# Kernel optimization log

Measured on AMD Instinct MI355X. Metric: run time of the kernel, lower is better.

Reference implementation:

```python
import jax, jax.numpy as jnp
import numpy as np

B, S, D = 4, 2048, 1024
H = 16
DH = D // H


def setup_inputs() -> dict:
    key = jax.random.key(0)
    ks = jax.random.split(key, 9)
    s = 0.02
    return {
        "x": jax.random.normal(ks[0], (B, S, D), dtype=jnp.float32),
        "Wq": jax.random.normal(ks[1], (D, D), dtype=jnp.float32) * s,
        "bq": jax.random.normal(ks[2], (D,), dtype=jnp.float32) * s,
        "Wk": jax.random.normal(ks[3], (D, D), dtype=jnp.float32) * s,
        "bk": jax.random.normal(ks[4], (D,), dtype=jnp.float32) * s,
        "Wv": jax.random.normal(ks[5], (D, D), dtype=jnp.float32) * s,
        "bv": jax.random.normal(ks[6], (D,), dtype=jnp.float32) * s,
        "Wo": jax.random.normal(ks[7], (D, D), dtype=jnp.float32) * s,
        "bo": jax.random.normal(ks[8], (D,), dtype=jnp.float32) * s,
    }


def _split_heads(t):
    # [B,S,D] -> [B,H,S,DH]
    b, s, d = t.shape
    return t.reshape(b, s, H, DH).transpose(0, 2, 1, 3)


def reference(x, Wq, bq, Wk, bk, Wv, bv, Wo, bo):
    q = _split_heads(x @ Wq.T + bq)
    k = _split_heads(x @ Wk.T + bk)
    v = _split_heads(x @ Wv.T + bv)
    scale = 1.0 / np.sqrt(DH).astype(np.float32)
    scores = jnp.einsum("bhqd,bhkd->bhqk", q, k) * scale  # [B,H,S,S]
    s = scores.shape[-2]
    causal = jnp.tril(jnp.ones((s, s), dtype=bool))
    scores = jnp.where(causal[None, None], scores, -jnp.inf)
    probs = jax.nn.softmax(scores, axis=-1)
    out = jnp.einsum("bhqk,bhkd->bhqd", probs, v)  # [B,H,S,DH]
    out = out.transpose(0, 2, 1, 3).reshape(x.shape[0], s, D)
    return out @ Wo.T + bo
```

## Files before the change

kernel.cpp:

```cpp
#include <hip/hip_runtime.h>
#include <hip/hip_bf16.h>
#include <cstdint>
#include <cstddef>


typedef unsigned short u16;
typedef __bf16 bf16x8 __attribute__((ext_vector_type(8)));
typedef float  f32x4  __attribute__((ext_vector_type(4)));

__device__ __forceinline__ u16 f2bf(float f) {
  unsigned u = __float_as_uint(f);
  unsigned r = u + 0x7fffu + ((u >> 16) & 1u);
  return (u16)(r >> 16);
}

__device__ __forceinline__ void llds16(const u16* g, u16* l) {
  __builtin_amdgcn_global_load_lds(
      (const __attribute__((address_space(1))) void*)g,
      (__attribute__((address_space(3))) void*)l, 16, 0, 0);
}

__global__ void cast_bf16_kernel(const float* __restrict__ in, u16* __restrict__ out, int n4) {
  int i = blockIdx.x * blockDim.x + threadIdx.x;
  if (i >= n4) return;
  float4 f = ((const float4*)in)[i];
  ushort4 u;
  u.x = f2bf(f.x); u.y = f2bf(f.y); u.z = f2bf(f.z); u.w = f2bf(f.w);
  ((ushort4*)out)[i] = u;
}

__global__ void cast4_kernel(const float* __restrict__ a, const float* __restrict__ b,
                             const float* __restrict__ c, const float* __restrict__ d,
                             u16* __restrict__ oa, u16* __restrict__ ob,
                             u16* __restrict__ oc, u16* __restrict__ od, int n4) {
  const int w = blockIdx.y;
  const float* src = (w == 0) ? a : (w == 1) ? b : (w == 2) ? c : d;
  u16* dst = (w == 0) ? oa : (w == 1) ? ob : (w == 2) ? oc : od;
  int i = blockIdx.x * blockDim.x + threadIdx.x;
  if (i >= n4) return;
  float4 f = ((const float4*)src)[i];
  ushort4 u;
  u.x = f2bf(f.x); u.y = f2bf(f.y); u.z = f2bf(f.z); u.w = f2bf(f.w);
  ((ushort4*)dst)[i] = u;
}

__global__ __launch_bounds__(256) void gemm_bt(
    const u16* __restrict__ A, const u16* __restrict__ Bw,
    const float* __restrict__ b0, const float* __restrict__ b1, const float* __restrict__ b2,
    u16* __restrict__ qkv_out, float* __restrict__ flat_out,
    int K, int mode)
{
  __shared__ u16 As[128 * 32];
  __shared__ u16 Bs[128 * 32];

  const int tid = threadIdx.x;
  const int n0 = blockIdx.x * 128;
  const int m0 = blockIdx.y * 128;

  const int srow = tid >> 2;
  const int soff = (tid & 3) * 8;
  const u16* gA0 = A  + (size_t)(m0 + srow) * K + soff;
  const u16* gA1 = gA0 + (size_t)64 * K;
  const u16* gB0 = Bw + (size_t)(n0 + srow) * K + soff;
  const u16* gB1 = gB0 + (size_t)64 * K;
  u16* lA0 = As + tid * 8;
  u16* lA1 = As + 2048 + tid * 8;
  u16* lB0 = Bs + tid * 8;
  u16* lB1 = Bs + 2048 + tid * 8;

  const int lane = tid & 63;
  const int wave = tid >> 6;
  const int wm = (wave >> 1) * 64;
  const int wn = (wave & 1) * 64;
  const int fr = lane & 15;
  const int k8 = (lane >> 4) * 8;

  f32x4 zero = {0.f, 0.f, 0.f, 0.f};
  f32x4 acc[4][4];
#pragma unroll
  for (int i = 0; i < 4; i++)
#pragma unroll
    for (int j = 0; j < 4; j++) acc[i][j] = zero;

  for (int k0 = 0; k0 < K; k0 += 32) {
    llds16(gA0 + k0, lA0);
    llds16(gA1 + k0, lA1);
    llds16(gB0 + k0, lB0);
    llds16(gB1 + k0, lB1);
    __syncthreads();
    bf16x8 af[4], bfr[4];
#pragma unroll
    for (int i = 0; i < 4; i++)
      af[i] = *(const bf16x8*)(As + (wm + i * 16 + fr) * 32 + k8);
#pragma unroll
    for (int j = 0; j < 4; j++)
      bfr[j] = *(const bf16x8*)(Bs + (wn + j * 16 + fr) * 32 + k8);
#pragma unroll
    for (int i = 0; i < 4; i++)
#pragma unroll
      for (int j = 0; j < 4; j++)
        acc[i][j] = __builtin_amdgcn_mfma_f32_16x16x32_bf16(af[i], bfr[j], acc[i][j], 0, 0, 0);
    __syncthreads();
  }

  const int rbase = (lane >> 4) * 4;
  if (mode == 0) {
    const int which = n0 >> 10;
    const float* bias = (which == 0) ? b0 : ((which == 1) ? b1 : b2);
    const float post = (which == 0) ? 0.18033688011f : 1.0f;
    u16* outb = qkv_out + (size_t)which * 8388608;
#pragma unroll
    for (int j = 0; j < 4; j++) {
      const int nn = (n0 + wn + j * 16 + fr) & 1023;
      const float bb = bias[nn];
      const int h = nn >> 6, dh = nn & 63;
#pragma unroll
      for (int i = 0; i < 4; i++) {
#pragma unroll
        for (int r = 0; r < 4; r++) {
          const int m = m0 + wm + i * 16 + rbase + r;
          const int bI = m >> 11, s = m & 2047;
          outb[(((size_t)bI * 16 + h) * 2048 + s) * 64 + dh] = f2bf((acc[i][j][r] + bb) * post);
        }
      }
    }
  } else {
#pragma unroll
    for (int j = 0; j < 4; j++) {
      const int n = n0 + wn + j * 16 + fr;
      const float bb = b0[n];
#pragma unroll
      for (int i = 0; i < 4; i++) {
#pragma unroll
        for (int r = 0; r < 4; r++) {
          const int m = m0 + wm + i * 16 + rbase + r;
          flat_out[(size_t)m * 1024 + n] = acc[i][j][r] + bb;
        }
      }
    }
  }
}

__global__ __launch_bounds__(256) void transpose_v(const u16* __restrict__ V, u16* __restrict__ VT) {
  __shared__ u16 t_s[64 * 72];
  const int tid = threadIdx.x;
  const int st = blockIdx.x << 6;
  const int bh = blockIdx.y;
  const u16* src = V + ((size_t)bh * 2048 + st) * 64;
#pragma unroll
  for (int p = 0; p < 2; p++) {
    int i = p * 256 + tid;
    int row = i >> 3, ch = i & 7;
    bf16x8 v = *(const bf16x8*)(src + row * 64 + ch * 8);
    *(bf16x8*)(t_s + row * 72 + ch * 8) = v;
  }
  __syncthreads();
  u16* dst = VT + (size_t)bh * 131072 + st;
#pragma unroll
  for (int p = 0; p < 2; p++) {
    int i = p * 256 + tid;
    int dh = i >> 3, ch = i & 7;
    union { u16 s[8]; bf16x8 v; } u;
#pragma unroll
    for (int e = 0; e < 8; e++) u.s[e] = t_s[(ch * 8 + e) * 72 + dh];
    *(bf16x8*)(dst + (size_t)dh * 2048 + ch * 8) = u.v;
  }
}

__global__ __launch_bounds__(256, 2) void attn_fa(
    const u16* __restrict__ Qb, const u16* __restrict__ Kb,
    const u16* __restrict__ VT, u16* __restrict__ Ob)
{
  __shared__ u16 k_s[2 * 4096];
  __shared__ u16 v_s[2 * 4096];
  __shared__ u16 p_s[2 * 9216];
  __shared__ float l_s[256];

  const int tid = threadIdx.x;
  const int lane = tid & 63;
  const int wave = tid >> 6;

  const int c = (int)blockIdx.x;
  const int xcd = c & 7;
  const int rr_ = c >> 3;
  const int bh = xcd + ((rr_ >> 3) << 3);
  const int pr = rr_ & 7;
  const int qtA = pr;
  const int qtB = 15 - pr;

  const size_t head = (size_t)bh << 17;
  const int fr = lane & 15;
  const int g = lane >> 4;
  const int k8 = g << 3;
  const int q0A = qtA << 7;
  const int q0B = qtB << 7;
  const int wrow = wave << 5;

  bf16x8 aqA[2][2], aqB[2][2];
#pragma unroll
  for (int f = 0; f < 2; f++) {
    const u16* qpA = Qb + head + (size_t)(q0A + wrow + (f << 4) + fr) * 64;
    aqA[f][0] = *(const bf16x8*)(qpA + k8);
    aqA[f][1] = *(const bf16x8*)(qpA + 32 + k8);
    const u16* qpB = Qb + head + (size_t)(q0B + wrow + (f << 4) + fr) * 64;
    aqB[f][0] = *(const bf16x8*)(qpB + k8);
    aqB[f][1] = *(const bf16x8*)(qpB + 32 + k8);
  }

  const int r0 = tid >> 3, c0 = tid & 7;
  const int r1 = 32 + r0;
  const int koff0 = r0 * 64 + (((c0 ^ r0) & 7) << 3);
  const int koff1 = r1 * 64 + (((c0 ^ r1) & 7) << 3);
  const int voff0 = r0 * 2048 + (((c0 ^ r0) & 7) << 3);
  const int voff1 = r1 * 2048 + (((c0 ^ r1) & 7) << 3);
  int kaddr[4][2], vaddr[2][4];
#pragma unroll
  for (int j = 0; j < 4; j++) {
    const int kn = (j << 4) + fr;
    kaddr[j][0] = kn * 64 + (((g ^ kn) & 7) << 3);
    kaddr[j][1] = kn * 64 + ((((g + 4) ^ kn) & 7) << 3);
#pragma unroll
    for (int s2 = 0; s2 < 2; s2++)
      vaddr[s2][j] = kn * 64 + ((((s2 << 2) + g) ^ (kn & 7)) << 3);
  }
  u16* const prowA0 = p_s + (wrow + fr) * 72;
  u16* const prowA1 = p_s + (wrow + 16 + fr) * 72;
  u16* const prowB0 = p_s + 9216 + (wrow + fr) * 72;
  u16* const prowB1 = p_s + 9216 + (wrow + 16 + fr) * 72;
  const u16* Kbase = Kb + head;
  const u16* Vbase = VT + head;

  auto issueK = [&](int jt2, int buf) {
    const u16* Kt = Kbase + ((size_t)jt2 << 12);
    llds16(Kt + koff0, k_s + (buf << 12) + tid * 8);
    llds16(Kt + koff1, k_s + (buf << 12) + 2048 + tid * 8);
  };
  auto issueV = [&](int jt2, int buf) {
    const u16* Vt = Vbase + (jt2 << 6);
    llds16(Vt + voff0, v_s + (buf << 12) + tid * 8);
    llds16(Vt + voff1, v_s + (buf << 12) + 2048 + tid * 8);
  };

  f32x4 oA[2][4], oB[2][4];
  const f32x4 zero = {0.f, 0.f, 0.f, 0.f};
#pragma unroll
  for (int f = 0; f < 2; f++)
#pragma unroll
    for (int j = 0; j < 4; j++) { oA[f][j] = zero; oB[f][j] = zero; }
  float lA[2] = {0.f, 0.f}, lB[2] = {0.f, 0.f};

  const int jmax = 2 * qtB + 1;
  const int diagA = 2 * qtA + (wave >> 1);
  const int diagB = 2 * qtB + (wave >> 1);

  auto do_pv = [&](const u16* vs, f32x4 (&oacc)[2][4], const u16* p0r, const u16* p1r) {
#pragma unroll
    for (int s2 = 0; s2 < 2; s2++) {
      const bf16x8 ap0 = *(const bf16x8*)(p0r + (s2 << 5) + k8);
      const bf16x8 ap1 = *(const bf16x8*)(p1r + (s2 << 5) + k8);
#pragma unroll
      for (int j = 0; j < 4; j++) {
        const bf16x8 bv = *(const bf16x8*)(vs + vaddr[s2][j]);
        oacc[0][j] = __builtin_amdgcn_mfma_f32_16x16x32_bf16(ap0, bv, oacc[0][j], 0, 0, 0);
        oacc[1][j] = __builtin_amdgcn_mfma_f32_16x16x32_bf16(ap1, bv, oacc[1][j], 0, 0, 0);
      }
    }
  };

  auto do_s = [&](const u16* ks, int jt, bool dodiag, int q0t,
                  const bf16x8 (&aqt)[2][2], float (&lr)[2], u16* p0r, u16* p1r) {
    f32x4 s_acc[2][4];
#pragma unroll
    for (int f = 0; f < 2; f++)
#pragma unroll
      for (int j = 0; j < 4; j++) s_acc[f][j] = zero;
#pragma unroll
    for (int j = 0; j < 4; j++) {
      const bf16x8 ka0 = *(const bf16x8*)(ks + kaddr[j][0]);
      const bf16x8 ka1 = *(const bf16x8*)(ks + kaddr[j][1]);
      s_acc[0][j] = __builtin_amdgcn_mfma_f32_16x16x32_bf16(ka0, aqt[0][0], s_acc[0][j], 0, 0, 0);
      s_acc[0][j] = __builtin_amdgcn_mfma_f32_16x16x32_bf16(ka1, aqt[0][1], s_acc[0][j], 0, 0, 0);
      s_acc[1][j] = __builtin_amdgcn_mfma_f32_16x16x32_bf16(ka0, aqt[1][0], s_acc[1][j], 0, 0, 0);
      s_acc[1][j] = __builtin_amdgcn_mfma_f32_16x16x32_bf16(ka1, aqt[1][1], s_acc[1][j], 0, 0, 0);
    }
#pragma unroll
    for (int f = 0; f < 2; f++) {
      const int qa = q0t + wrow + (f << 4) + fr;
      u16* prow = (f == 0) ? p0r : p1r;
      if (dodiag) {
#pragma unroll
        for (int j = 0; j < 4; j++) {
          const int ka = (jt << 6) + (j << 4) + (g << 2);
          float p0 = (ka + 0 > qa) ? 0.f : __builtin_amdgcn_exp2f(s_acc[f][j][0]);
          float p1 = (ka + 1 > qa) ? 0.f : __builtin_amdgcn_exp2f(s_acc[f][j][1]);
          float p2 = (ka + 2 > qa) ? 0.f : __builtin_amdgcn_exp2f(s_acc[f][j][2]);
          float p3 = (ka + 3 > qa) ? 0.f : __builtin_amdgcn_exp2f(s_acc[f][j][3]);
          lr[f] += (p0 + p1) + (p2 + p3);
          union { __hip_bfloat162 h; unsigned u; } ca, cb;
          ca.h = __float22bfloat162_rn(make_float2(p0, p1));
          cb.h = __float22bfloat162_rn(make_float2(p2, p3));
          *(uint2*)(prow + (j << 4) + (g << 2)) = make_uint2(ca.u, cb.u);
        }
      } else {
#pragma unroll
        for (int j = 0; j < 4; j++) {
          float p0 = __builtin_amdgcn_exp2f(s_acc[f][j][0]);
          float p1 = __builtin_amdgcn_exp2f(s_acc[f][j][1]);
          float p2 = __builtin_amdgcn_exp2f(s_acc[f][j][2]);
          float p3 = __builtin_amdgcn_exp2f(s_acc[f][j][3]);
          lr[f] += (p0 + p1) + (p2 + p3);
          union { __hip_bfloat162 h; unsigned u; } ca, cb;
          ca.h = __float22bfloat162_rn(make_float2(p0, p1));
          cb.h = __float22bfloat162_rn(make_float2(p2, p3));
          *(uint2*)(prow + (j << 4) + (g << 2)) = make_uint2(ca.u, cb.u);
        }
      }
    }
  };

  issueK(0, 0);

  for (int jt = 0; jt <= jmax; jt++) {
    const int buf = jt & 1;
    __syncthreads();
    if (jt < jmax) issueK(jt + 1, buf ^ 1);
    issueV(jt, buf);
    if (jt > 0) {
      const u16* vprev = v_s + ((buf ^ 1) << 12);
      if (jt - 1 <= diagB) do_pv(vprev, oB, prowB0, prowB1);
      if (jt - 1 <= diagA) do_pv(vprev, oA, prowA0, prowA1);
    }
    if (jt <= diagB) do_s(k_s + (buf << 12), jt, jt == diagB, q0B, aqB, lB, prowB0, prowB1);
    if (jt <= diagA) do_s(k_s + (buf << 12), jt, jt == diagA, q0A, aqA, lA, prowA0, prowA1);
  }
  __syncthreads();
  if (diagB == jmax) do_pv(v_s + ((jmax & 1) << 12), oB, prowB0, prowB1);

#pragma unroll
  for (int f = 0; f < 2; f++) {
    float la = lA[f];
    la += __shfl_xor(la, 16);
    la += __shfl_xor(la, 32);
    if (g == 0) l_s[wrow + (f << 4) + fr] = la;
    float lb = lB[f];
    lb += __shfl_xor(lb, 16);
    lb += __shfl_xor(lb, 32);
    if (g == 0) l_s[128 + wrow + (f << 4) + fr] = lb;
  }
  const int b = bh >> 4, h = bh & 15;
#pragma unroll
  for (int f = 0; f < 2; f++) {
#pragma unroll
    for (int r = 0; r < 4; r++) {
      const int qloc = wrow + (f << 4) + (g << 2) + r;
      const float invA = 1.f / l_s[qloc];
      const float invB = 1.f / l_s[128 + qloc];
      const int qA_abs = q0A + qloc;
      const int qB_abs = q0B + qloc;
#pragma unroll
      for (int j = 0; j < 4; j++) {
        Ob[((size_t)b * 2048 + qA_abs) * 1024 + (h << 6) + (j << 4) + fr] =
            f2bf(oA[f][j][r] * invA);
        Ob[((size_t)b * 2048 + qB_abs) * 1024 + (h << 6) + (j << 4) + fr] =
            f2bf(oB[f][j][r] * invB);
      }
    }
  }
}

extern "C" void kernel_launch(void* const* d_in, const int* in_sizes, int n_in,
                              void* d_out, int out_size, void* d_ws, size_t ws_size,
                              hipStream_t stream) {
  const float* x  = (const float*)d_in[0];
  const float* Wq = (const float*)d_in[1];
  const float* bq = (const float*)d_in[2];
  const float* Wk = (const float*)d_in[3];
  const float* bk = (const float*)d_in[4];
  const float* Wv = (const float*)d_in[5];
  const float* bv = (const float*)d_in[6];
  const float* Wo = (const float*)d_in[7];
  const float* bo = (const float*)d_in[8];
  float* out = (float*)d_out;

  char* ws = (char*)d_ws;
  u16* xb    = (u16*)(ws);
  u16* vT    = (u16*)(ws);
  u16* wqkv  = (u16*)(ws + 16777216);
  u16* wo    = (u16*)(ws + 23068672);
  u16* qkv   = (u16*)(ws + 25165824);
  u16* attnb = (u16*)(ws + 75497472);

  cast_bf16_kernel<<<8192, 256, 0, stream>>>(x, xb, 2097152);
  cast4_kernel<<<dim3(1024, 4), 256, 0, stream>>>(
      Wq, Wk, Wv, Wo, wqkv, wqkv + 1048576, wqkv + 2097152, wo, 262144);

  gemm_bt<<<dim3(24, 64), 256, 0, stream>>>(xb, wqkv, bq, bk, bv, qkv, nullptr, 1024, 0);

  transpose_v<<<dim3(32, 64), 256, 0, stream>>>(qkv + 16777216, vT);

  attn_fa<<<dim3(512), 256, 0, stream>>>(qkv, qkv + 8388608, vT, attnb);

  gemm_bt<<<dim3(8, 64), 256, 0, stream>>>(attnb, wo, bo, bo, bo, nullptr, out, 1024, 1);
}
```

Before: 285.3 us.

## Replace QKV projection GEMM with 256x256-tile, 8-wave pipelined kernel

```diff
diff --git a/kernel.cpp b/kernel.cpp
--- a/kernel.cpp
+++ b/kernel.cpp
@@ -44,6 +44,171 @@
   ((ushort4*)dst)[i] = u;
 }
 
+__global__ __launch_bounds__(512, 2) void gemm_qkv_256(
+    const u16* __restrict__ A, const u16* __restrict__ Bw,
+    const float* __restrict__ b0, const float* __restrict__ b1, const float* __restrict__ b2,
+    u16* __restrict__ qkv_out)
+{
+  __shared__ u16 lds[65536];
+
+  const int tid = threadIdx.x;
+  const int lane = tid & 63;
+  const int wave = tid >> 6;
+
+  const int bid = (int)blockIdx.x;
+  const int c2 = (bid & 7) * 48 + (bid >> 3);
+  const int mt = c2 / 12;
+  const int nt = c2 - mt * 12;
+  const int m0 = mt << 8;
+  const int n0 = nt << 8;
+
+  const int warp_m = wave >> 2;
+  const int warp_n = wave & 3;
+  const int wm = warp_m << 7;
+  const int wn = warp_n << 6;
+  const int fr = lane & 15;
+  const int g  = lane >> 4;
+
+  const int srow = tid >> 3;
+  const int schk = ((tid & 7) ^ (srow & 7)) << 3;
+  const u16* pA = A  + (size_t)(m0 + srow) * 1024 + schk;
+  const u16* pB = Bw + (size_t)(n0 + srow) * 1024 + schk;
+
+  const int rsw0 = ((g    ) ^ (fr & 7)) << 3;
+  const int rsw1 = ((g ^ 4) ^ (fr & 7)) << 3;
+
+  const u16* Ab0 = lds + warp_m * 8192 + fr * 64;
+  const u16* Bb0 = lds + 16384 + (warp_n >> 1) * 8192 + (warp_n & 1) * 4096 + fr * 64;
+  const u16* Ab1 = Ab0 + 32768;
+  const u16* Bb1 = Bb0 + 32768;
+
+  f32x4 acc[8][4];
+  const f32x4 zero = {0.f, 0.f, 0.f, 0.f};
+#pragma unroll
+  for (int i = 0; i < 8; i++)
+#pragma unroll
+    for (int j = 0; j < 4; j++) acc[i][j] = zero;
+
+  bf16x8 a_[4][2];
+  bf16x8 b_[4][2];
+
+  auto stage = [&](int kt, int buf, int matBoff, int half, const u16* psrc) {
+    const u16* src = psrc + (size_t)half * 131072 + (kt << 6);
+    u16* dst = lds + buf * 32768 + matBoff + half * 8192 + tid * 8;
+    llds16(src, dst);
+    llds16(src + 65536, dst + 4096);
+  };
+  auto loadA = [&](const u16* Ab, int ib) {
+#pragma unroll
+    for (int ii = 0; ii < 4; ii++) {
+      const u16* r = Ab + (ib + ii) * 1024;
+      a_[ii][0] = *(const bf16x8*)(r + rsw0);
+      a_[ii][1] = *(const bf16x8*)(r + rsw1);
+    }
+  };
+  auto loadB2 = [&](const u16* Bb, int jb) {
+#pragma unroll
+    for (int jj = 0; jj < 2; jj++) {
+      const u16* r = Bb + (jb + jj) * 1024;
+      b_[jb + jj][0] = *(const bf16x8*)(r + rsw0);
+      b_[jb + jj][1] = *(const bf16x8*)(r + rsw1);
+    }
+  };
+  auto mfma8 = [&](int ib, int jb) {
+    __builtin_amdgcn_s_setprio(1);
+#pragma unroll
+    for (int jj = 0; jj < 2; jj++)
+#pragma unroll
+      for (int ii = 0; ii < 4; ii++) {
+        acc[ib+ii][jb+jj] = __builtin_amdgcn_mfma_f32_16x16x32_bf16(
+            a_[ii][0], b_[jb+jj][0], acc[ib+ii][jb+jj], 0, 0, 0);
+        acc[ib+ii][jb+jj] = __builtin_amdgcn_mfma_f32_16x16x32_bf16(
+            a_[ii][1], b_[jb+jj][1], acc[ib+ii][jb+jj], 0, 0, 0);
+      }
+    __builtin_amdgcn_s_setprio(0);
+  };
+
+  stage(0, 0, 0,     0, pA);
+  stage(0, 0, 0,     1, pA);
+  stage(0, 0, 16384, 0, pB);
+  stage(0, 0, 16384, 1, pB);
+  stage(1, 1, 0,     0, pA);
+  asm volatile("s_waitcnt vmcnt(2)" ::: "memory");
+  __builtin_amdgcn_s_barrier();
+
+  const int NTI = 8;
+  for (int t = 0; t < NTI; ++t) {
+    const bool st = (t < NTI - 1);
+    const int ka = 2 * t + 1;
+    const int kb = 2 * t + 2;
+    const int kc = 2 * t + 3;
+
+    loadA(Ab0, 0); loadB2(Bb0, 0);
+    stage(ka, 1, 0, 1, pA);
+    __builtin_amdgcn_s_barrier();
+    mfma8(0, 0);
+    __builtin_amdgcn_s_barrier();
+    loadB2(Bb0, 2);
+    stage(ka, 1, 16384, 0, pB);
+    __builtin_amdgcn_s_barrier();
+    mfma8(0, 2);
+    __builtin_amdgcn_s_barrier();
+    loadA(Ab0, 4);
+    stage(ka, 1, 16384, 1, pB);
+    __builtin_amdgcn_s_barrier();
+    mfma8(4, 2);
+    __builtin_amdgcn_s_barrier();
+    if (st) stage(kb, 0, 0, 0, pA);
+    __builtin_amdgcn_s_barrier();
+    mfma8(4, 0);
+    if (st) { asm volatile("s_waitcnt vmcnt(2)" ::: "memory"); }
+    else    { asm volatile("s_waitcnt vmcnt(0)" ::: "memory"); }
+    __builtin_amdgcn_s_barrier();
+
+    loadA(Ab1, 0); loadB2(Bb1, 0);
+    if (st) stage(kb, 0, 0, 1, pA);
+    __builtin_amdgcn_s_barrier();
+    mfma8(0, 0);
+    __builtin_amdgcn_s_barrier();
+    loadB2(Bb1, 2);
+    if (st) stage(kb, 0, 16384, 0, pB);
+    __builtin_amdgcn_s_barrier();
+    mfma8(0, 2);
+    __builtin_amdgcn_s_barrier();
+    loadA(Ab1, 4);
+    if (st) stage(kb, 0, 16384, 1, pB);
+    __builtin_amdgcn_s_barrier();
+    mfma8(4, 2);
+    __builtin_amdgcn_s_barrier();
+    if (st) stage(kc, 1, 0, 0, pA);
+    __builtin_amdgcn_s_barrier();
+    mfma8(4, 0);
+    if (st) { asm volatile("s_waitcnt vmcnt(2)" ::: "memory"); }
+    __builtin_amdgcn_s_barrier();
+  }
+
+  const int rbase = g * 4;
+  const int which = n0 >> 10;
+  const float* bias = (which == 0) ? b0 : ((which == 1) ? b1 : b2);
+  const float post = (which == 0) ? 0.18033688011f : 1.0f;
+  u16* outb = qkv_out + (size_t)which * 8388608;
+#pragma unroll
+  for (int j = 0; j < 4; j++) {
+    const int nn = (n0 + wn + j * 16 + fr) & 1023;
+    const float bb = bias[nn];
+    const int h = nn >> 6, dh = nn & 63;
+#pragma unroll
+    for (int i = 0; i < 8; i++) {
+#pragma unroll
+      for (int r = 0; r < 4; r++) {
+        const int m = m0 + wm + i * 16 + rbase + r;
+        const int bI = m >> 11, s = m & 2047;
+        outb[(((size_t)bI * 16 + h) * 2048 + s) * 64 + dh] = f2bf((acc[i][j][r] + bb) * post);
+      }
+    }
+  }
+}
+
 __global__ __launch_bounds__(256) void gemm_bt(
     const u16* __restrict__ A, const u16* __restrict__ Bw,
     const float* __restrict__ b0, const float* __restrict__ b1, const float* __restrict__ b2,
@@ -394,7 +559,7 @@
   cast4_kernel<<<dim3(1024, 4), 256, 0, stream>>>(
       Wq, Wk, Wv, Wo, wqkv, wqkv + 1048576, wqkv + 2097152, wo, 262144);
 
-  gemm_bt<<<dim3(24, 64), 256, 0, stream>>>(xb, wqkv, bq, bk, bv, qkv, nullptr, 1024, 0);
+  gemm_qkv_256<<<dim3(384), 512, 0, stream>>>(xb, wqkv, bq, bk, bv, qkv);
 
   transpose_v<<<dim3(32, 64), 256, 0, stream>>>(qkv + 16777216, vT);
 
```

After: 269.2 us. 5.6% less time.
